# Kernel optimization log

Hardware: AMD Instinct MI355X
Metric: run time of the kernel (lower is better)

## Reference

```python
import jax, jax.numpy as jnp
import numpy as np

E, H, I = 8, 1024, 1024  # num_local_experts, hidden_size, intermediate_size
T = 4096                 # tokens (batch*seq)
ALPHA, LIMIT = 1.702, 7.0


def setup_inputs() -> dict:
    key = jax.random.key(0)
    ks = jax.random.split(key, 6)
    return {
        "hidden_states": jax.random.normal(ks[0], (T, H), dtype=jnp.float32),
        "routing_weights": jax.random.uniform(ks[1], (T, E), dtype=jnp.float32),
        "gate_up_proj": jax.random.normal(ks[2], (E, H, 2 * I), dtype=jnp.float32) * 0.02,
        "gate_up_proj_bias": jax.random.normal(ks[3], (E, 2 * I), dtype=jnp.float32) * 0.02,
        "down_proj": jax.random.normal(ks[4], (E, H, I), dtype=jnp.float32) * 0.02,
        "down_proj_bias": jax.random.normal(ks[5], (E, I), dtype=jnp.float32) * 0.02,
    }


def reference(hidden_states, routing_weights, gate_up_proj, gate_up_proj_bias,
              down_proj, down_proj_bias):
    # Dense all-experts path (GPT-OSS Experts forward).
    # gate_up: [E, T, 2I]
    gate_up = jnp.einsum('th,ehf->etf', hidden_states, gate_up_proj) + gate_up_proj_bias[:, None, :]
    gate = gate_up[..., ::2]   # interleaved split
    up = gate_up[..., 1::2]
    gate = jnp.minimum(gate, LIMIT)
    up = jnp.clip(up, -LIMIT, LIMIT)
    glu = gate * jax.nn.sigmoid(gate * ALPHA)
    act = (up + 1.0) * glu     # [E, T, I]
    # down_proj declared [E, H, I] -> contract over I
    out_e = jnp.einsum('eti,ehi->eth', act, down_proj) + down_proj_bias[:, None, :]  # [E, T, H]
    out = jnp.einsum('eth,te->th', out_e, routing_weights)  # [T, H]
    return out
```

## Files before the change

kernel.cpp:

```cpp
#include <hip/hip_runtime.h>
#include <hip/hip_bf16.h>
#include <stdint.h>

#define T_DIM 4096
#define H_DIM 1024
#define I_DIM 1024
#define E_DIM 8
#define F_DIM 2048
#define K2_DIM 8192
#define ALPHA_C 1.702f
#define LIMIT_C 7.0f

typedef unsigned short u16;
typedef __bf16 bf8 __attribute__((ext_vector_type(8)));
typedef float f4 __attribute__((ext_vector_type(4)));

__device__ __forceinline__ u16 f2bf(float f) {
  union { float f; unsigned u; } x; x.f = f;
  unsigned r = (x.u + 0x7fffu + ((x.u >> 16) & 1u)) >> 16;
  return (u16)r;
}

__device__ __forceinline__ void gload16(const void* g, void* l) {
  __builtin_amdgcn_global_load_lds(
      (const __attribute__((address_space(1))) void*)g,
      (__attribute__((address_space(3))) void*)l,
      16, 0, 0);
}


__global__ void cast_bf16_kernel(const float* __restrict__ in, u16* __restrict__ out, int n4) {
  int idx = blockIdx.x * blockDim.x + threadIdx.x;
  int stride = gridDim.x * blockDim.x;
  for (int i = idx; i < n4; i += stride) {
    float4 v = reinterpret_cast<const float4*>(in)[i];
    ushort4 o;
    o.x = f2bf(v.x); o.y = f2bf(v.y); o.z = f2bf(v.z); o.w = f2bf(v.w);
    reinterpret_cast<ushort4*>(out)[i] = o;
  }
}

__global__ void cast_transpose_gup(const float* __restrict__ in, u16* __restrict__ out) {
  __shared__ float tile[32][33];
  int e = blockIdx.z, h0 = blockIdx.y * 32, f0 = blockIdx.x * 32;
  int tx = threadIdx.x & 31, ty = threadIdx.x >> 5;
  const float* src = in + (size_t)e * H_DIM * F_DIM;
  u16* dst = out + (size_t)e * F_DIM * H_DIM;
#pragma unroll
  for (int r = ty; r < 32; r += 8) tile[r][tx] = src[(size_t)(h0 + r) * F_DIM + f0 + tx];
  __syncthreads();
#pragma unroll
  for (int r = ty; r < 32; r += 8) dst[(size_t)(f0 + r) * H_DIM + h0 + tx] = f2bf(tile[tx][r]);
}

__global__ void bias_init(const float* __restrict__ rw, const float* __restrict__ db,
                          float* __restrict__ out) {
  __shared__ float db_s[E_DIM][H_DIM];
  for (int i = threadIdx.x; i < E_DIM * H_DIM; i += 256)
    db_s[i >> 10][i & 1023] = db[i];
  int t = blockIdx.x;
  float r0[E_DIM];
#pragma unroll
  for (int e = 0; e < E_DIM; ++e) r0[e] = rw[(size_t)t * E_DIM + e];
  __syncthreads();
  for (int h = threadIdx.x; h < H_DIM; h += 256) {
    float s = 0.f;
#pragma unroll
    for (int e = 0; e < E_DIM; ++e) s += r0[e] * db_s[e][h];
    out[(size_t)t * H_DIM + h] = s;
  }
}


__global__ __launch_bounds__(256, 2) void gemm1_act(
    const u16* __restrict__ A,
    const u16* __restrict__ Bt,
    const float* __restrict__ rw,
    const float* __restrict__ gbias,
    u16* __restrict__ act2)
{
  const int e  = blockIdx.z;
  const int t0 = blockIdx.y * 128;
  const int n0 = blockIdx.x * 128;
  const int tid = threadIdx.x;
  const int w = tid >> 6, l = tid & 63;
  const int wr = w >> 1, wc = w & 1;

  __shared__ u16 As[128 * 32];
  __shared__ u16 Bs[128 * 32];
  __shared__ float rw_s[128];
  __shared__ float gb_s[128];

  if (tid < 128) {
    rw_s[tid] = rw[(size_t)(t0 + tid) * E_DIM + e];
    gb_s[tid] = gbias[(size_t)e * F_DIM + n0 + tid];
  }

  const u16* bBase = Bt + (size_t)e * F_DIM * H_DIM;

  f4 acc[4][4];
#pragma unroll
  for (int m = 0; m < 4; ++m)
#pragma unroll
    for (int n = 0; n < 4; ++n) acc[m][n] = f4{0.f, 0.f, 0.f, 0.f};

  const int row_st = l >> 2;
  const int col_sw = (((l & 3) ^ ((l >> 3) & 3)) * 8);

  for (int kt = 0; kt < H_DIM / 32; ++kt) {
    const int k0 = kt * 32;
    __syncthreads();
#pragma unroll
    for (int c = 0; c < 2; ++c) {
      int q = w * 2 + c;
      int row = q * 16 + row_st;
      gload16(A + (size_t)(t0 + row) * H_DIM + k0 + col_sw, (char*)As + q * 1024);
      gload16(bBase + (size_t)(n0 + row) * H_DIM + k0 + col_sw, (char*)Bs + q * 1024);
    }
    __syncthreads();

    bf8 af[4], bfr[4];
#pragma unroll
    for (int m = 0; m < 4; ++m) {
      int row = wr * 64 + m * 16 + (l & 15);
      int ch = (l >> 4) ^ ((row >> 1) & 3);
      af[m] = *(const bf8*)(As + row * 32 + ch * 8);
    }
#pragma unroll
    for (int n = 0; n < 4; ++n) {
      int row = wc * 64 + n * 16 + (l & 15);
      int ch = (l >> 4) ^ ((row >> 1) & 3);
      bfr[n] = *(const bf8*)(Bs + row * 32 + ch * 8);
    }
#pragma unroll
    for (int m = 0; m < 4; ++m)
#pragma unroll
      for (int n = 0; n < 4; ++n)
        acc[m][n] = __builtin_amdgcn_mfma_f32_16x16x32_bf16(af[m], bfr[n], acc[m][n], 0, 0, 0);
  }

#pragma unroll
  for (int m = 0; m < 4; ++m) {
#pragma unroll
    for (int n = 0; n < 4; ++n) {
#pragma unroll
      for (int r = 0; r < 4; ++r) {
        int row = wr * 64 + m * 16 + (l >> 4) * 4 + r;
        int col = wc * 64 + n * 16 + (l & 15);
        float v = acc[m][n][r] + gb_s[col];
        float o = __shfl_xor(v, 1, 64);
        float gate = (l & 1) ? o : v;
        float up   = (l & 1) ? v : o;
        gate = fminf(gate, LIMIT_C);
        up   = fminf(fmaxf(up, -LIMIT_C), LIMIT_C);
        float glu = gate / (1.f + __expf(-gate * ALPHA_C));
        float a = (up + 1.f) * glu * rw_s[row];
        if (!(l & 1)) {
          int i = (n0 + col) >> 1;
          act2[(size_t)(t0 + row) * K2_DIM + e * I_DIM + i] = f2bf(a);
        }
      }
    }
  }
}


__global__ __launch_bounds__(256, 2) void gemm2(
    const u16* __restrict__ A,
    const u16* __restrict__ Bt,
    float* __restrict__ out)
{
  const int t0 = blockIdx.y * 128;
  const int n0 = blockIdx.x * 128;
  const int s  = blockIdx.z;
  const int tid = threadIdx.x;
  const int w = tid >> 6, l = tid & 63;
  const int wr = w >> 1, wc = w & 1;

  __shared__ u16 As[128 * 32];
  __shared__ u16 Bs[128 * 32];

  f4 acc[4][4];
#pragma unroll
  for (int m = 0; m < 4; ++m)
#pragma unroll
    for (int n = 0; n < 4; ++n) acc[m][n] = f4{0.f, 0.f, 0.f, 0.f};

  const int row_st = l >> 2;
  const int col_sw = (((l & 3) ^ ((l >> 3) & 3)) * 8);

  const int kt_beg = s * (K2_DIM / 32 / 4);
  const int kt_end = kt_beg + (K2_DIM / 32 / 4);
  for (int kt = kt_beg; kt < kt_end; ++kt) {
    const int k0 = kt * 32;
    const int eb = k0 >> 10;
    const int ki = k0 & 1023;
    __syncthreads();
#pragma unroll
    for (int c = 0; c < 2; ++c) {
      int q = w * 2 + c;
      int row = q * 16 + row_st;
      gload16(A + (size_t)(t0 + row) * K2_DIM + k0 + col_sw, (char*)As + q * 1024);
      gload16(Bt + ((size_t)eb * H_DIM + n0 + row) * I_DIM + ki + col_sw, (char*)Bs + q * 1024);
    }
    __syncthreads();

    bf8 af[4], bfr[4];
#pragma unroll
    for (int m = 0; m < 4; ++m) {
      int row = wr * 64 + m * 16 + (l & 15);
      int ch = (l >> 4) ^ ((row >> 1) & 3);
      af[m] = *(const bf8*)(As + row * 32 + ch * 8);
    }
#pragma unroll
    for (int n = 0; n < 4; ++n) {
      int row = wc * 64 + n * 16 + (l & 15);
      int ch = (l >> 4) ^ ((row >> 1) & 3);
      bfr[n] = *(const bf8*)(Bs + row * 32 + ch * 8);
    }
#pragma unroll
    for (int m = 0; m < 4; ++m)
#pragma unroll
      for (int n = 0; n < 4; ++n)
        acc[m][n] = __builtin_amdgcn_mfma_f32_16x16x32_bf16(af[m], bfr[n], acc[m][n], 0, 0, 0);
  }

#pragma unroll
  for (int m = 0; m < 4; ++m) {
#pragma unroll
    for (int n = 0; n < 4; ++n) {
#pragma unroll
      for (int r = 0; r < 4; ++r) {
        int row = wr * 64 + m * 16 + (l >> 4) * 4 + r;
        int col = wc * 64 + n * 16 + (l & 15);
        atomicAdd(out + (size_t)(t0 + row) * H_DIM + n0 + col, acc[m][n][r]);
      }
    }
  }
}


extern "C" void kernel_launch(void* const* d_in, const int* in_sizes, int n_in,
                              void* d_out, int out_size, void* d_ws, size_t ws_size,
                              hipStream_t stream) {
  const float* hs  = (const float*)d_in[0];
  const float* rw  = (const float*)d_in[1];
  const float* gup = (const float*)d_in[2];
  const float* gub = (const float*)d_in[3];
  const float* dp  = (const float*)d_in[4];
  const float* db  = (const float*)d_in[5];
  float* out = (float*)d_out;
  char* ws = (char*)d_ws;

  u16* hs_bf = (u16*)(ws);
  u16* gupT  = (u16*)(ws + 8ll  * 1024 * 1024);
  u16* dp_bf = (u16*)(ws + 40ll * 1024 * 1024);
  u16* act2  = (u16*)(ws + 56ll * 1024 * 1024);

  cast_bf16_kernel<<<2048, 256, 0, stream>>>(hs, hs_bf, T_DIM * H_DIM / 4);
  cast_transpose_gup<<<dim3(F_DIM / 32, H_DIM / 32, E_DIM), 256, 0, stream>>>(gup, gupT);
  cast_bf16_kernel<<<2048, 256, 0, stream>>>(dp, dp_bf, E_DIM * H_DIM * I_DIM / 4);
  bias_init<<<T_DIM, 256, 0, stream>>>(rw, db, out);
  gemm1_act<<<dim3(F_DIM / 128, T_DIM / 128, E_DIM), 256, 0, stream>>>(hs_bf, gupT, rw, gub, act2);
  gemm2<<<dim3(H_DIM / 128, T_DIM / 128, 4), 256, 0, stream>>>(act2, dp_bf, out);
}
```

Measured before the change: 491.9 us.

## Rewrite both GEMMs as 256x256 double-buffered 8-wave pipelined kernels

Both GEMM kernels move from 128x128 tiles with 4 waves and a load, sync, compute loop to 256x256 tiles with 8 waves. The new loop uses a K=64 step with double-buffered LDS (128KB) and splits each iteration into four compute phases. Each phase interleaves its global-to-LDS loads with the MFMAs, using explicit vmcnt waits, barriers and setprio. The aim is to hide memory latency and raise reuse per loaded byte, at the cost of large LDS use that likely allows only one block per CU despite launch_bounds(512,2), and fewer blocks in gemm2 (128).

```diff
diff --git a/kernel.cpp b/kernel.cpp
--- a/kernel.cpp
+++ b/kernel.cpp
@@ -15,6 +15,12 @@
 typedef __bf16 bf8 __attribute__((ext_vector_type(8)));
 typedef float f4 __attribute__((ext_vector_type(4)));
 
+#define MFMA16(d, va, vb) d = __builtin_amdgcn_mfma_f32_16x16x32_bf16(va, vb, d, 0, 0, 0)
+#define VMW(n) asm volatile("s_waitcnt vmcnt(" #n ")" ::: "memory")
+#define LGKM0 asm volatile("s_waitcnt lgkmcnt(0)" ::: "memory")
+#define SBAR __builtin_amdgcn_s_barrier()
+#define SCHED0 __builtin_amdgcn_sched_barrier(0)
+
 __device__ __forceinline__ u16 f2bf(float f) {
   union { float f; unsigned u; } x; x.f = f;
   unsigned r = (x.u + 0x7fffu + ((x.u >> 16) & 1u)) >> 16;
@@ -72,92 +78,143 @@
 }
 
 
-__global__ __launch_bounds__(256, 2) void gemm1_act(
+__global__ __launch_bounds__(512, 2) void gemm1_act8(
     const u16* __restrict__ A,
     const u16* __restrict__ Bt,
     const float* __restrict__ rw,
     const float* __restrict__ gbias,
     u16* __restrict__ act2)
 {
+  __shared__ __align__(16) u16 ldsbuf[65536];
   const int e  = blockIdx.z;
-  const int t0 = blockIdx.y * 128;
-  const int n0 = blockIdx.x * 128;
+  const int t0 = blockIdx.y * 256;
+  const int n0 = blockIdx.x * 256;
   const int tid = threadIdx.x;
-  const int w = tid >> 6, l = tid & 63;
-  const int wr = w >> 1, wc = w & 1;
-
-  __shared__ u16 As[128 * 32];
-  __shared__ u16 Bs[128 * 32];
-  __shared__ float rw_s[128];
-  __shared__ float gb_s[128];
-
-  if (tid < 128) {
-    rw_s[tid] = rw[(size_t)(t0 + tid) * E_DIM + e];
-    gb_s[tid] = gbias[(size_t)e * F_DIM + n0 + tid];
-  }
-
-  const u16* bBase = Bt + (size_t)e * F_DIM * H_DIM;
-
-  f4 acc[4][4];
-#pragma unroll
-  for (int m = 0; m < 4; ++m)
-#pragma unroll
-    for (int n = 0; n < 4; ++n) acc[m][n] = f4{0.f, 0.f, 0.f, 0.f};
-
-  const int row_st = l >> 2;
-  const int col_sw = (((l & 3) ^ ((l >> 3) & 3)) * 8);
-
-  for (int kt = 0; kt < H_DIM / 32; ++kt) {
-    const int k0 = kt * 32;
-    __syncthreads();
-#pragma unroll
-    for (int c = 0; c < 2; ++c) {
-      int q = w * 2 + c;
-      int row = q * 16 + row_st;
-      gload16(A + (size_t)(t0 + row) * H_DIM + k0 + col_sw, (char*)As + q * 1024);
-      gload16(bBase + (size_t)(n0 + row) * H_DIM + k0 + col_sw, (char*)Bs + q * 1024);
-    }
-    __syncthreads();
-
-    bf8 af[4], bfr[4];
+  const int l = tid & 63, w = tid >> 6;
+  const int wm = w >> 2, wn = w & 3;
+
+  const int g = tid >> 3, cl = tid & 7;
+  int ra[4] = { g, 128 + g, 64 + g, 192 + g };
+  int rbb = (g & 31) + ((g >> 5) << 6);
+  int rb[4] = { rbb, 128 + rbb, 32 + rbb, 160 + rbb };
+  const u16* gA[4]; const u16* gB[4]; int dA[4], dB[4];
+  const u16* bB = Bt + (size_t)e * F_DIM * H_DIM;
+#pragma unroll
+  for (int j = 0; j < 4; ++j) {
+    gA[j] = A + (size_t)(t0 + ra[j]) * H_DIM + (cl ^ ((ra[j] >> 1) & 7)) * 8;
+    dA[j] = ra[j] * 64 + cl * 8;
+    gB[j] = bB + (size_t)(n0 + rb[j]) * H_DIM + (cl ^ ((rb[j] >> 1) & 7)) * 8;
+    dB[j] = 16384 + rb[j] * 64 + cl * 8;
+  }
+
+  const int lr = l & 15, qq = l >> 4, sw = (l >> 1) & 7;
+  const int ks0 = (qq ^ sw) * 8, ks1 = ((4 + qq) ^ sw) * 8;
+  const int aRow = (wm * 128 + lr) * 64;
+  const int bRow = 16384 + (wn * 64 + lr) * 64;
+
+  f4 acc[8][4];
+#pragma unroll
+  for (int i = 0; i < 8; ++i)
+#pragma unroll
+    for (int j = 0; j < 4; ++j) acc[i][j] = f4{0.f, 0.f, 0.f, 0.f};
+
+  gload16(gA[0], ldsbuf + dA[0]); gload16(gA[1], ldsbuf + dA[1]);
+  gload16(gB[0], ldsbuf + dB[0]); gload16(gB[1], ldsbuf + dB[1]);
+  gload16(gB[2], ldsbuf + dB[2]); gload16(gB[3], ldsbuf + dB[3]);
+  gload16(gA[2], ldsbuf + dA[2]); gload16(gA[3], ldsbuf + dA[3]);
+  VMW(4);
+  SBAR;
+
+  bf8 af[4][2], b0[2][2], b1[2][2];
+  const int NT = H_DIM / 64;
+  for (int t = 0; t < NT; ++t) {
+    const u16* L = ldsbuf + (t & 1) * 32768;
+    u16* S = ldsbuf + ((t + 1) & 1) * 32768;
+    const bool st = (t + 1 < NT);
+    const int ka = (t + 1) * 64;
 #pragma unroll
     for (int m = 0; m < 4; ++m) {
-      int row = wr * 64 + m * 16 + (l & 15);
-      int ch = (l >> 4) ^ ((row >> 1) & 3);
-      af[m] = *(const bf8*)(As + row * 32 + ch * 8);
-    }
-#pragma unroll
-    for (int n = 0; n < 4; ++n) {
-      int row = wc * 64 + n * 16 + (l & 15);
-      int ch = (l >> 4) ^ ((row >> 1) & 3);
-      bfr[n] = *(const bf8*)(Bs + row * 32 + ch * 8);
-    }
-#pragma unroll
-    for (int m = 0; m < 4; ++m)
-#pragma unroll
-      for (int n = 0; n < 4; ++n)
-        acc[m][n] = __builtin_amdgcn_mfma_f32_16x16x32_bf16(af[m], bfr[n], acc[m][n], 0, 0, 0);
-  }
-
-#pragma unroll
-  for (int m = 0; m < 4; ++m) {
-#pragma unroll
-    for (int n = 0; n < 4; ++n) {
-#pragma unroll
-      for (int r = 0; r < 4; ++r) {
-        int row = wr * 64 + m * 16 + (l >> 4) * 4 + r;
-        int col = wc * 64 + n * 16 + (l & 15);
-        float v = acc[m][n][r] + gb_s[col];
+      af[m][0] = *(const bf8*)(L + aRow + m * 1024 + ks0);
+      af[m][1] = *(const bf8*)(L + aRow + m * 1024 + ks1);
+    }
+#pragma unroll
+    for (int n = 0; n < 2; ++n) {
+      b0[n][0] = *(const bf8*)(L + bRow + n * 1024 + ks0);
+      b0[n][1] = *(const bf8*)(L + bRow + n * 1024 + ks1);
+    }
+    if (st) { gload16(gA[0] + ka, S + dA[0]); gload16(gA[1] + ka, S + dA[1]); VMW(4); }
+    else VMW(2);
+    SBAR; LGKM0; SCHED0;
+    __builtin_amdgcn_s_setprio(1);
+#pragma unroll
+    for (int n = 0; n < 2; ++n)
+#pragma unroll
+      for (int m = 0; m < 4; ++m) { MFMA16(acc[m][n], af[m][0], b0[n][0]); MFMA16(acc[m][n], af[m][1], b0[n][1]); }
+    __builtin_amdgcn_s_setprio(0);
+    SBAR;
+#pragma unroll
+    for (int n = 0; n < 2; ++n) {
+      b1[n][0] = *(const bf8*)(L + bRow + (2 + n) * 1024 + ks0);
+      b1[n][1] = *(const bf8*)(L + bRow + (2 + n) * 1024 + ks1);
+    }
+    if (st) { gload16(gB[0] + ka, S + dB[0]); gload16(gB[1] + ka, S + dB[1]); VMW(4); }
+    else VMW(0);
+    SBAR; LGKM0; SCHED0;
+    __builtin_amdgcn_s_setprio(1);
+#pragma unroll
+    for (int n = 0; n < 2; ++n)
+#pragma unroll
+      for (int m = 0; m < 4; ++m) { MFMA16(acc[m][2 + n], af[m][0], b1[n][0]); MFMA16(acc[m][2 + n], af[m][1], b1[n][1]); }
+    __builtin_amdgcn_s_setprio(0);
+    SBAR;
+#pragma unroll
+    for (int m = 0; m < 4; ++m) {
+      af[m][0] = *(const bf8*)(L + aRow + (4 + m) * 1024 + ks0);
+      af[m][1] = *(const bf8*)(L + aRow + (4 + m) * 1024 + ks1);
+    }
+    if (st) { gload16(gB[2] + ka, S + dB[2]); gload16(gB[3] + ka, S + dB[3]); VMW(4); }
+    SBAR; LGKM0; SCHED0;
+    __builtin_amdgcn_s_setprio(1);
+#pragma unroll
+    for (int n = 0; n < 2; ++n)
+#pragma unroll
+      for (int m = 0; m < 4; ++m) { MFMA16(acc[4 + m][2 + n], af[m][0], b1[n][0]); MFMA16(acc[4 + m][2 + n], af[m][1], b1[n][1]); }
+    __builtin_amdgcn_s_setprio(0);
+    SBAR;
+    if (st) { gload16(gA[2] + ka, S + dA[2]); gload16(gA[3] + ka, S + dA[3]); VMW(4); }
+    SBAR; LGKM0; SCHED0;
+    __builtin_amdgcn_s_setprio(1);
+#pragma unroll
+    for (int n = 0; n < 2; ++n)
+#pragma unroll
+      for (int m = 0; m < 4; ++m) { MFMA16(acc[4 + m][n], af[m][0], b0[n][0]); MFMA16(acc[4 + m][n], af[m][1], b0[n][1]); }
+    __builtin_amdgcn_s_setprio(0);
+    SBAR;
+  }
+
+  float gbv[4];
+#pragma unroll
+  for (int n = 0; n < 4; ++n)
+    gbv[n] = gbias[(size_t)e * F_DIM + n0 + wn * 64 + n * 16 + lr];
+#pragma unroll
+  for (int m = 0; m < 8; ++m) {
+#pragma unroll
+    for (int r = 0; r < 4; ++r) {
+      int row = wm * 128 + m * 16 + qq * 4 + r;
+      float rwv = rw[(size_t)(t0 + row) * E_DIM + e];
+#pragma unroll
+      for (int n = 0; n < 4; ++n) {
+        float v = acc[m][n][r] + gbv[n];
         float o = __shfl_xor(v, 1, 64);
         float gate = (l & 1) ? o : v;
         float up   = (l & 1) ? v : o;
         gate = fminf(gate, LIMIT_C);
         up   = fminf(fmaxf(up, -LIMIT_C), LIMIT_C);
         float glu = gate / (1.f + __expf(-gate * ALPHA_C));
-        float a = (up + 1.f) * glu * rw_s[row];
+        float a = (up + 1.f) * glu * rwv;
         if (!(l & 1)) {
-          int i = (n0 + col) >> 1;
-          act2[(size_t)(t0 + row) * K2_DIM + e * I_DIM + i] = f2bf(a);
+          int col = wn * 64 + n * 16 + lr;
+          act2[(size_t)(t0 + row) * K2_DIM + e * I_DIM + ((n0 + col) >> 1)] = f2bf(a);
         }
       }
     }
@@ -165,78 +222,133 @@
 }
 
 
-__global__ __launch_bounds__(256, 2) void gemm2(
+__global__ __launch_bounds__(512, 2) void gemm2_8(
     const u16* __restrict__ A,
-    const u16* __restrict__ Bt,
+    const u16* __restrict__ dp,
     float* __restrict__ out)
 {
-  const int t0 = blockIdx.y * 128;
-  const int n0 = blockIdx.x * 128;
+  __shared__ __align__(16) u16 ldsbuf[65536];
   const int s  = blockIdx.z;
+  const int t0 = blockIdx.y * 256;
+  const int n0 = blockIdx.x * 256;
   const int tid = threadIdx.x;
-  const int w = tid >> 6, l = tid & 63;
-  const int wr = w >> 1, wc = w & 1;
-
-  __shared__ u16 As[128 * 32];
-  __shared__ u16 Bs[128 * 32];
-
-  f4 acc[4][4];
-#pragma unroll
-  for (int m = 0; m < 4; ++m)
-#pragma unroll
-    for (int n = 0; n < 4; ++n) acc[m][n] = f4{0.f, 0.f, 0.f, 0.f};
-
-  const int row_st = l >> 2;
-  const int col_sw = (((l & 3) ^ ((l >> 3) & 3)) * 8);
-
-  const int kt_beg = s * (K2_DIM / 32 / 4);
-  const int kt_end = kt_beg + (K2_DIM / 32 / 4);
-  for (int kt = kt_beg; kt < kt_end; ++kt) {
-    const int k0 = kt * 32;
-    const int eb = k0 >> 10;
-    const int ki = k0 & 1023;
-    __syncthreads();
-#pragma unroll
-    for (int c = 0; c < 2; ++c) {
-      int q = w * 2 + c;
-      int row = q * 16 + row_st;
-      gload16(A + (size_t)(t0 + row) * K2_DIM + k0 + col_sw, (char*)As + q * 1024);
-      gload16(Bt + ((size_t)eb * H_DIM + n0 + row) * I_DIM + ki + col_sw, (char*)Bs + q * 1024);
-    }
-    __syncthreads();
-
-    bf8 af[4], bfr[4];
+  const int l = tid & 63, w = tid >> 6;
+  const int wm = w >> 2, wn = w & 3;
+
+  const int g = tid >> 3, cl = tid & 7;
+  int ra[4] = { g, 128 + g, 64 + g, 192 + g };
+  int rbb = (g & 31) + ((g >> 5) << 6);
+  int rb[4] = { rbb, 128 + rbb, 32 + rbb, 160 + rbb };
+  const u16* gA[4]; size_t rpB[4]; int dA[4], dB[4];
+#pragma unroll
+  for (int j = 0; j < 4; ++j) {
+    gA[j] = A + (size_t)(t0 + ra[j]) * K2_DIM + s * 2048 + (cl ^ ((ra[j] >> 1) & 7)) * 8;
+    dA[j] = ra[j] * 64 + cl * 8;
+    rpB[j] = (size_t)(n0 + rb[j]) * I_DIM + (cl ^ ((rb[j] >> 1) & 7)) * 8;
+    dB[j] = 16384 + rb[j] * 64 + cl * 8;
+  }
+
+  const int lr = l & 15, qq = l >> 4, sw = (l >> 1) & 7;
+  const int ks0 = (qq ^ sw) * 8, ks1 = ((4 + qq) ^ sw) * 8;
+  const int aRow = (wm * 128 + lr) * 64;
+  const int bRow = 16384 + (wn * 64 + lr) * 64;
+
+  f4 acc[8][4];
+#pragma unroll
+  for (int i = 0; i < 8; ++i)
+#pragma unroll
+    for (int j = 0; j < 4; ++j) acc[i][j] = f4{0.f, 0.f, 0.f, 0.f};
+
+  {
+    const u16* bT = dp + (size_t)(s * 2) * (H_DIM * I_DIM);
+    gload16(gA[0], ldsbuf + dA[0]); gload16(gA[1], ldsbuf + dA[1]);
+    gload16(bT + rpB[0], ldsbuf + dB[0]); gload16(bT + rpB[1], ldsbuf + dB[1]);
+    gload16(bT + rpB[2], ldsbuf + dB[2]); gload16(bT + rpB[3], ldsbuf + dB[3]);
+    gload16(gA[2], ldsbuf + dA[2]); gload16(gA[3], ldsbuf + dA[3]);
+  }
+  VMW(4);
+  SBAR;
+
+  bf8 af[4][2], b0[2][2], b1[2][2];
+  const int NT = 2048 / 64;
+  for (int t = 0; t < NT; ++t) {
+    const u16* L = ldsbuf + (t & 1) * 32768;
+    u16* S = ldsbuf + ((t + 1) & 1) * 32768;
+    const bool st = (t + 1 < NT);
+    const int ka = (t + 1) * 64;
+    const int kk = s * 2048 + ka;
+    const u16* bT = dp + (size_t)(kk >> 10) * (H_DIM * I_DIM) + (kk & 1023);
 #pragma unroll
     for (int m = 0; m < 4; ++m) {
-      int row = wr * 64 + m * 16 + (l & 15);
-      int ch = (l >> 4) ^ ((row >> 1) & 3);
-      af[m] = *(const bf8*)(As + row * 32 + ch * 8);
-    }
-#pragma unroll
-    for (int n = 0; n < 4; ++n) {
-      int row = wc * 64 + n * 16 + (l & 15);
-      int ch = (l >> 4) ^ ((row >> 1) & 3);
-      bfr[n] = *(const bf8*)(Bs + row * 32 + ch * 8);
-    }
-#pragma unroll
-    for (int m = 0; m < 4; ++m)
-#pragma unroll
-      for (int n = 0; n < 4; ++n)
-        acc[m][n] = __builtin_amdgcn_mfma_f32_16x16x32_bf16(af[m], bfr[n], acc[m][n], 0, 0, 0);
-  }
-
-#pragma unroll
-  for (int m = 0; m < 4; ++m) {
-#pragma unroll
-    for (int n = 0; n < 4; ++n) {
-#pragma unroll
-      for (int r = 0; r < 4; ++r) {
-        int row = wr * 64 + m * 16 + (l >> 4) * 4 + r;
-        int col = wc * 64 + n * 16 + (l & 15);
+      af[m][0] = *(const bf8*)(L + aRow + m * 1024 + ks0);
+      af[m][1] = *(const bf8*)(L + aRow + m * 1024 + ks1);
+    }
+#pragma unroll
+    for (int n = 0; n < 2; ++n) {
+      b0[n][0] = *(const bf8*)(L + bRow + n * 1024 + ks0);
+      b0[n][1] = *(const bf8*)(L + bRow + n * 1024 + ks1);
+    }
+    if (st) { gload16(gA[0] + ka, S + dA[0]); gload16(gA[1] + ka, S + dA[1]); VMW(4); }
+    else VMW(2);
+    SBAR; LGKM0; SCHED0;
+    __builtin_amdgcn_s_setprio(1);
+#pragma unroll
+    for (int n = 0; n < 2; ++n)
+#pragma unroll
+      for (int m = 0; m < 4; ++m) { MFMA16(acc[m][n], af[m][0], b0[n][0]); MFMA16(acc[m][n], af[m][1], b0[n][1]); }
+    __builtin_amdgcn_s_setprio(0);
+    SBAR;
+#pragma unroll
+    for (int n = 0; n < 2; ++n) {
+      b1[n][0] = *(const bf8*)(L + bRow + (2 + n) * 1024 + ks0);
+      b1[n][1] = *(const bf8*)(L + bRow + (2 + n) * 1024 + ks1);
+    }
+    if (st) { gload16(bT + rpB[0], S + dB[0]); gload16(bT + rpB[1], S + dB[1]); VMW(4); }
+    else VMW(0);
+    SBAR; LGKM0; SCHED0;
+    __builtin_amdgcn_s_setprio(1);
+#pragma unroll
+    for (int n = 0; n < 2; ++n)
+#pragma unroll
+      for (int m = 0; m < 4; ++m) { MFMA16(acc[m][2 + n], af[m][0], b1[n][0]); MFMA16(acc[m][2 + n], af[m][1], b1[n][1]); }
+    __builtin_amdgcn_s_setprio(0);
+    SBAR;
+#pragma unroll
+    for (int m = 0; m < 4; ++m) {
+      af[m][0] = *(const bf8*)(L + aRow + (4 + m) * 1024 + ks0);
+      af[m][1] = *(const bf8*)(L + aRow + (4 + m) * 1024 + ks1);
+    }
+    if (st) { gload16(bT + rpB[2], S + dB[2]); gload16(bT + rpB[3], S + dB[3]); VMW(4); }
+    SBAR; LGKM0; SCHED0;
+    __builtin_amdgcn_s_setprio(1);
+#pragma unroll
+    for (int n = 0; n < 2; ++n)
+#pragma unroll
+      for (int m = 0; m < 4; ++m) { MFMA16(acc[4 + m][2 + n], af[m][0], b1[n][0]); MFMA16(acc[4 + m][2 + n], af[m][1], b1[n][1]); }
+    __builtin_amdgcn_s_setprio(0);
+    SBAR;
+    if (st) { gload16(gA[2] + ka, S + dA[2]); gload16(gA[3] + ka, S + dA[3]); VMW(4); }
+    SBAR; LGKM0; SCHED0;
+    __builtin_amdgcn_s_setprio(1);
+#pragma unroll
+    for (int n = 0; n < 2; ++n)
+#pragma unroll
+      for (int m = 0; m < 4; ++m) { MFMA16(acc[4 + m][n], af[m][0], b0[n][0]); MFMA16(acc[4 + m][n], af[m][1], b0[n][1]); }
+    __builtin_amdgcn_s_setprio(0);
+    SBAR;
+  }
+
+#pragma unroll
+  for (int m = 0; m < 8; ++m)
+#pragma unroll
+    for (int r = 0; r < 4; ++r) {
+      int row = wm * 128 + m * 16 + qq * 4 + r;
+#pragma unroll
+      for (int n = 0; n < 4; ++n) {
+        int col = wn * 64 + n * 16 + lr;
         atomicAdd(out + (size_t)(t0 + row) * H_DIM + n0 + col, acc[m][n][r]);
       }
     }
-  }
 }
 
 
@@ -261,6 +373,6 @@
   cast_transpose_gup<<<dim3(F_DIM / 32, H_DIM / 32, E_DIM), 256, 0, stream>>>(gup, gupT);
   cast_bf16_kernel<<<2048, 256, 0, stream>>>(dp, dp_bf, E_DIM * H_DIM * I_DIM / 4);
   bias_init<<<T_DIM, 256, 0, stream>>>(rw, db, out);
-  gemm1_act<<<dim3(F_DIM / 128, T_DIM / 128, E_DIM), 256, 0, stream>>>(hs_bf, gupT, rw, gub, act2);
-  gemm2<<<dim3(H_DIM / 128, T_DIM / 128, 4), 256, 0, stream>>>(act2, dp_bf, out);
-}
+  gemm1_act8<<<dim3(F_DIM / 256, T_DIM / 256, E_DIM), 512, 0, stream>>>(hs_bf, gupT, rw, gub, act2);
+  gemm2_8<<<dim3(H_DIM / 256, T_DIM / 256, 4), 512, 0, stream>>>(act2, dp_bf, out);
+}
```

New measurement: 466.9 us. 5.1% less time.
